# Performance work log

Measured on AMD Instinct MI355X. Metric: run time of the kernel, lower is better.

Reference implementation:

```python
import jax, jax.numpy as jnp
import numpy as np

D_IN, D, P, H, DH, DFF, L = 3072, 1024, 36, 8, 128, 2048, 6
SCALE = np.float32(1.0 / np.sqrt(DH))
# leave-one-out index matrix: row i lists all patch indices except i -> (36, 35)
LOO_IDX = jnp.asarray(np.array([[j for j in range(P) if j != i] for i in range(P)], dtype=np.int32))


def _ln(x, g, b, eps=1e-5):
    m = jnp.mean(x, axis=-1, keepdims=True)
    v = jnp.var(x, axis=-1, keepdims=True)
    return (x - m) / jnp.sqrt(v + eps) * g + b


def setup_inputs() -> dict:
    key = jax.random.key(0)
    ks = jax.random.split(key, 16)
    w = lambda k, shape: jax.random.normal(k, shape, jnp.float32) * 0.02
    return {
        "x": jax.random.normal(ks[0], (128, P, D_IN), jnp.float32),
        "ln0_g": jnp.ones((D_IN,), jnp.float32), "ln0_b": jnp.zeros((D_IN,), jnp.float32),
        "Wred": w(ks[1], (D, D_IN)), "bred": jnp.zeros((D,), jnp.float32),
        "h0_w1": w(ks[2], (64, D)), "h0_b1": jnp.zeros((64,), jnp.float32),
        "h0_w2": w(ks[3], (1, 64)), "h0_b2": jnp.zeros((1,), jnp.float32),
        "temperature": jnp.ones((1,), jnp.float32) * 0.07,
        "Wqkv": w(ks[4], (L, 3 * D, D)), "bqkv": jnp.zeros((L, 3 * D), jnp.float32),
        "Wo": w(ks[5], (L, D, D)), "bo": jnp.zeros((L, D), jnp.float32),
        "ln1_g": jnp.ones((L, D), jnp.float32), "ln1_b": jnp.zeros((L, D), jnp.float32),
        "W1": w(ks[6], (L, DFF, D)), "b1": jnp.zeros((L, DFF), jnp.float32),
        "W2": w(ks[7], (L, D, DFF)), "b2": jnp.zeros((L, D), jnp.float32),
        "ln2_g": jnp.ones((L, D), jnp.float32), "ln2_b": jnp.zeros((L, D), jnp.float32),
        "lnf_g": jnp.ones((D,), jnp.float32), "lnf_b": jnp.zeros((D,), jnp.float32),
    }


def reference(x, ln0_g, ln0_b, Wred, bred, h0_w1, h0_b1, h0_w2, h0_b2, temperature,
              Wqkv, bqkv, Wo, bo, ln1_g, ln1_b, W1, b1, W2, b2, ln2_g, ln2_b, lnf_g, lnf_b):
    B = x.shape[0]
    # dim_reduce (dropout is identity at inference)
    xr = jax.nn.gelu(_ln(x, ln0_g, ln0_b) @ Wred.T + bred, approximate=False)  # (B,P,D)

    # Leave-one-out attention maps. H0 is a pointwise (kernel_size=1) stack,
    # so each position's score is independent: compute once, then gather the
    h1 = jax.nn.gelu(jnp.einsum('bpc,oc->bpo', xr, h0_w1) + h0_b1, approximate=False)  # (B,P,64)
    full = jnp.einsum('bpo,uo->bpu', h1, h0_w2)[..., 0] + h0_b2[0]                      # (B,P)
    attention_maps = jax.nn.sigmoid(full[:, LOO_IDX] / temperature[0])                  # (B,P,P-1)

    # Pre-norm transformer encoder (PyTorch norm_first=True, relu FFN, no final encoder norm)
    y = xr
    for l in range(L):
        qkv = _ln(y, ln1_g[l], ln1_b[l]) @ Wqkv[l].T + bqkv[l]  # (B,P,3D)
        q, k, v = jnp.split(qkv, 3, axis=-1)
        q = q.reshape(B, P, H, DH).transpose(0, 2, 1, 3)
        k = k.reshape(B, P, H, DH).transpose(0, 2, 1, 3)
        v = v.reshape(B, P, H, DH).transpose(0, 2, 1, 3)
        attn = jax.nn.softmax(jnp.einsum('bhqd,bhkd->bhqk', q, k) * SCALE, axis=-1)
        o = jnp.einsum('bhqk,bhkd->bhqd', attn, v).transpose(0, 2, 1, 3).reshape(B, P, D)
        y = y + o @ Wo[l].T + bo[l]
        f = jax.nn.relu(_ln(y, ln2_g[l], ln2_b[l]) @ W1[l].T + b1[l])
        y = y + f @ W2[l].T + b2[l]

    return _ln(y, lnf_g, lnf_b), attention_maps
```

## Files before the change

kernel.cpp:

```cpp
#include <hip/hip_runtime.h>
#include <hip/hip_bf16.h>

typedef unsigned short u16;
typedef unsigned int u32;
typedef __bf16 bf16x8 __attribute__((ext_vector_type(8)));
typedef float f32x4 __attribute__((ext_vector_type(4)));

#define DEV static __device__ __forceinline__
#define GPTR(p) (const __attribute__((address_space(1))) u32*)(p)
#define LPTR(p) (__attribute__((address_space(3))) u32*)(p)

DEV float bf2f(u16 u) { return __uint_as_float((u32)u << 16); }
DEV u16 f2bf(float f) {
  u32 x = __float_as_uint(f);
  x += 0x7fffu + ((x >> 16) & 1u);
  return (u16)(x >> 16);
}
DEV float gelu_f(float x) { return 0.5f * x * (1.0f + erff(x * 0.70710678118654752440f)); }

__global__ void cvt_k(const float* __restrict__ in, u16* __restrict__ out, int n4) {
  int i = blockIdx.x * 256 + threadIdx.x;
  if (i < n4) {
    float4 v = ((const float4*)in)[i];
    ushort4 o;
    o.x = f2bf(v.x); o.y = f2bf(v.y); o.z = f2bf(v.z); o.w = f2bf(v.w);
    ((ushort4*)out)[i] = o;
  }
}

__global__ void w1t_k(const float* __restrict__ w1, float* __restrict__ w1t) {
  int i = blockIdx.x * 256 + threadIdx.x;
  if (i < 64 * 1024) {
    int o = i >> 10, c = i & 1023;
    w1t[c * 64 + o] = w1[i];
  }
}

template<int DIM, int OUTM>
__global__ __launch_bounds__(256) void ln_k(const float* __restrict__ in,
                                            const float* __restrict__ g,
                                            const float* __restrict__ b,
                                            void* __restrict__ outp) {
  constexpr int NV = DIM / 1024;
  const int row = blockIdx.x, tid = threadIdx.x;
  const float* x = in + (size_t)row * DIM;
  float4 v[NV];
  float s = 0.f, s2 = 0.f;
#pragma unroll
  for (int i = 0; i < NV; ++i) {
    v[i] = ((const float4*)x)[tid + i * 256];
    s += v[i].x + v[i].y + v[i].z + v[i].w;
    s2 += v[i].x * v[i].x + v[i].y * v[i].y + v[i].z * v[i].z + v[i].w * v[i].w;
  }
  __shared__ float red[8];
#pragma unroll
  for (int off = 32; off; off >>= 1) { s += __shfl_down(s, off); s2 += __shfl_down(s2, off); }
  if ((tid & 63) == 0) { red[(tid >> 6) * 2] = s; red[(tid >> 6) * 2 + 1] = s2; }
  __syncthreads();
  s = red[0] + red[2] + red[4] + red[6];
  s2 = red[1] + red[3] + red[5] + red[7];
  const float mean = s / DIM;
  const float rstd = rsqrtf(s2 / DIM - mean * mean + 1e-5f);
#pragma unroll
  for (int i = 0; i < NV; ++i) {
    const int c4 = tid + i * 256;
    float4 gv = ((const float4*)g)[c4];
    float4 bv = ((const float4*)b)[c4];
    float o0 = (v[i].x - mean) * rstd * gv.x + bv.x;
    float o1 = (v[i].y - mean) * rstd * gv.y + bv.y;
    float o2 = (v[i].z - mean) * rstd * gv.z + bv.z;
    float o3 = (v[i].w - mean) * rstd * gv.w + bv.w;
    if (OUTM == 0) {
      ushort4 u4;
      u4.x = f2bf(o0); u4.y = f2bf(o1); u4.z = f2bf(o2); u4.w = f2bf(o3);
      ((ushort4*)outp)[(size_t)row * (DIM / 4) + c4] = u4;
    } else {
      ((float4*)outp)[(size_t)row * (DIM / 4) + c4] = make_float4(o0, o1, o2, o3);
    }
  }
}

template<int EPI, int BN>
__global__ __launch_bounds__(512, 4) void gemm_bt(const u16* __restrict__ A,
                                                  const u16* __restrict__ B,
                                                  const float* __restrict__ bias,
                                                  float* __restrict__ Cf,
                                                  u16* __restrict__ Cb,
                                                  int N, int K, int nx) {
  constexpr int WC = BN / 32;
  constexpr int MR = (128 * WC / 8) / 16;
  __shared__ u16 As[2][128 * 64];
  __shared__ u16 Bs[2][BN * 64];
  const int tid = threadIdx.x;
  const int nwg = gridDim.x;
  const int bid = blockIdx.x;
  const int swz = (bid & 7) * (nwg >> 3) + (bid >> 3);
  const int by = swz / nx, bx = swz - by * nx;
  const int brow = by * 128, bcol = bx * BN;
  const int lane = tid & 63, w = tid >> 6;
  const int wr = (w / WC) * (MR * 16), wc = (w % WC) * 32;
  const int fr = lane & 15, fg = lane >> 4;
  const int swb = (fr & 7) << 4;
  const int ldr = lane >> 3;
  const int lc8 = lane & 7;
  const int cs8 = (lc8 ^ ldr) * 8;

  const u16* Ab = A + (size_t)(brow + ldr) * K + cs8;
  const u16* Bb = B + (size_t)(bcol + ldr) * K + cs8;

  f32x4 acc[MR][2];
  const f32x4 z = {0.f, 0.f, 0.f, 0.f};
#pragma unroll
  for (int m = 0; m < MR; ++m) { acc[m][0] = z; acc[m][1] = z; }

  auto stage = [&](int kt, int buf) {
    const int k0 = kt << 6;
#pragma unroll
    for (int i = 0; i < 2; ++i) {
      const int c = i * 8 + w;
      __builtin_amdgcn_global_load_lds(GPTR(Ab + (size_t)c * 8 * K + k0),
                                       LPTR(&As[buf][c * 512 + lane * 8]), 16, 0, 0);
    }
#pragma unroll
    for (int i = 0; i < BN / 64; ++i) {
      const int c = i * 8 + w;
      __builtin_amdgcn_global_load_lds(GPTR(Bb + (size_t)c * 8 * K + k0),
                                       LPTR(&Bs[buf][c * 512 + lane * 8]), 16, 0, 0);
    }
  };

  stage(0, 0);
  const int nkt = K >> 6;
  for (int kt = 0; kt < nkt; ++kt) {
    const int buf = kt & 1;
    asm volatile("s_waitcnt vmcnt(0)" ::: "memory");
    __builtin_amdgcn_s_barrier();
    __builtin_amdgcn_sched_barrier(0);
    if (kt + 1 < nkt) stage(kt + 1, buf ^ 1);
    const char* Asb = (const char*)&As[buf][0];
    const char* Bsb = (const char*)&Bs[buf][0];
    __builtin_amdgcn_s_setprio(1);
#pragma unroll
    for (int ks = 0; ks < 2; ++ks) {
      bf16x8 af[MR], bfr[2];
      const int cb = (ks * 64 + fg * 16) ^ swb;
#pragma unroll
      for (int m = 0; m < MR; ++m)
        af[m] = *(const bf16x8*)(Asb + (wr + m * 16 + fr) * 128 + cb);
#pragma unroll
      for (int n = 0; n < 2; ++n)
        bfr[n] = *(const bf16x8*)(Bsb + (wc + n * 16 + fr) * 128 + cb);
#pragma unroll
      for (int m = 0; m < MR; ++m)
#pragma unroll
        for (int n = 0; n < 2; ++n)
          acc[m][n] = __builtin_amdgcn_mfma_f32_16x16x32_bf16(af[m], bfr[n], acc[m][n], 0, 0, 0);
    }
    __builtin_amdgcn_s_setprio(0);
  }

#pragma unroll
  for (int n = 0; n < 2; ++n) {
    const int col = bcol + wc + n * 16 + fr;
    const float bv = bias[col];
#pragma unroll
    for (int m = 0; m < MR; ++m) {
      const int row0 = brow + wr + m * 16 + fg * 4;
#pragma unroll
      for (int j = 0; j < 4; ++j) {
        float v = acc[m][n][j] + bv;
        const size_t idx = (size_t)(row0 + j) * N + col;
        if (EPI == 0) Cf[idx] = gelu_f(v);
        else if (EPI == 1) Cb[idx] = f2bf(v);
        else if (EPI == 2) Cf[idx] = Cf[idx] + v;
        else Cb[idx] = f2bf(fmaxf(v, 0.f));
      }
    }
  }
}

__global__ __launch_bounds__(256) void attn_k(const u16* __restrict__ qkv, u16* __restrict__ o) {
  constexpr int LDQ = 136;
  __shared__ u16 Q[36 * LDQ], Kk[36 * LDQ], V[36 * LDQ];
  __shared__ float S[36][38];
  const int tid = threadIdx.x;
  const int b = blockIdx.x >> 3, h = blockIdx.x & 7;
  const size_t base = (size_t)b * 36 * 3072 + h * 128;
  for (int i = tid; i < 36 * 16; i += 256) {
    const int r = i >> 4, c = (i & 15) << 3;
    const size_t src = base + (size_t)r * 3072 + c;
    *(uint4*)&Q[r * LDQ + c] = *(const uint4*)&qkv[src];
    *(uint4*)&Kk[r * LDQ + c] = *(const uint4*)&qkv[src + 1024];
    *(uint4*)&V[r * LDQ + c] = *(const uint4*)&qkv[src + 2048];
  }
  __syncthreads();
  for (int i = tid; i < 36 * 36; i += 256) {
    const int r = i / 36, c = i - r * 36;
    float s = 0.f;
    for (int d = 0; d < 128; ++d) s += bf2f(Q[r * LDQ + d]) * bf2f(Kk[c * LDQ + d]);
    S[r][c] = s * 0.08838834764831845f;
  }
  __syncthreads();
  if (tid < 36) {
    float mx = -1e30f;
    for (int c = 0; c < 36; ++c) mx = fmaxf(mx, S[tid][c]);
    float sum = 0.f;
    for (int c = 0; c < 36; ++c) { float e = expf(S[tid][c] - mx); S[tid][c] = e; sum += e; }
    const float inv = 1.f / sum;
    for (int c = 0; c < 36; ++c) S[tid][c] *= inv;
  }
  __syncthreads();
  for (int i = tid; i < 36 * 16; i += 256) {
    const int r = i >> 4, d0 = (i & 15) << 3;
    float s[8] = {0.f, 0.f, 0.f, 0.f, 0.f, 0.f, 0.f, 0.f};
    for (int j = 0; j < 36; ++j) {
      const float p = S[r][j];
#pragma unroll
      for (int e = 0; e < 8; ++e) s[e] += p * bf2f(V[j * LDQ + d0 + e]);
    }
    uint4 pk;
    pk.x = (u32)f2bf(s[0]) | ((u32)f2bf(s[1]) << 16);
    pk.y = (u32)f2bf(s[2]) | ((u32)f2bf(s[3]) << 16);
    pk.z = (u32)f2bf(s[4]) | ((u32)f2bf(s[5]) << 16);
    pk.w = (u32)f2bf(s[6]) | ((u32)f2bf(s[7]) << 16);
    *(uint4*)&o[(size_t)(b * 36 + r) * 1024 + h * 128 + d0] = pk;
  }
}

__global__ __launch_bounds__(256) void h0_k(const float* __restrict__ xr,
                                            const float* __restrict__ w1t,
                                            const float* __restrict__ b1,
                                            const float* __restrict__ w2,
                                            const float* __restrict__ b2v,
                                            float* __restrict__ full) {
  __shared__ float xs[1024];
  __shared__ float hp[4][64];
  const int token = blockIdx.x, tid = threadIdx.x;
  ((float4*)xs)[tid] = ((const float4*)(xr + (size_t)token * 1024))[tid];
  __syncthreads();
  const int w = tid >> 6, lane = tid & 63;
  float s = 0.f;
  const int c0 = w * 256;
  for (int c = c0; c < c0 + 256; ++c) s += xs[c] * w1t[c * 64 + lane];
  hp[w][lane] = s;
  __syncthreads();
  if (tid < 64) {
    float h = hp[0][tid] + hp[1][tid] + hp[2][tid] + hp[3][tid] + b1[tid];
    h = gelu_f(h);
    float v = h * w2[tid];
#pragma unroll
    for (int off = 32; off; off >>= 1) v += __shfl_down(v, off);
    if (tid == 0) full[token] = v + b2v[0];
  }
}

__global__ void am2_k(const float* __restrict__ full, const float* __restrict__ temp,
                      float* __restrict__ out) {
  const int i = blockIdx.x * 256 + threadIdx.x;
  if (i < 128 * 36 * 35) {
    const int j = i % 35;
    const int t = i / 35;
    const int p = t % 36;
    const int b = t / 36;
    const int col = j + (j >= p ? 1 : 0);
    const float v = full[b * 36 + col] / temp[0];
    out[i] = 1.f / (1.f + expf(-v));
  }
}

extern "C" void kernel_launch(void* const* d_in, const int* in_sizes, int n_in,
                              void* d_out, int out_size, void* d_ws, size_t ws_size,
                              hipStream_t stream) {
  const float* x     = (const float*)d_in[0];
  const float* ln0_g = (const float*)d_in[1];
  const float* ln0_b = (const float*)d_in[2];
  const float* Wred  = (const float*)d_in[3];
  const float* bred  = (const float*)d_in[4];
  const float* h0_w1 = (const float*)d_in[5];
  const float* h0_b1 = (const float*)d_in[6];
  const float* h0_w2 = (const float*)d_in[7];
  const float* h0_b2 = (const float*)d_in[8];
  const float* temp  = (const float*)d_in[9];
  const float* Wqkv  = (const float*)d_in[10];
  const float* bqkv  = (const float*)d_in[11];
  const float* Wo    = (const float*)d_in[12];
  const float* bo    = (const float*)d_in[13];
  const float* ln1_g = (const float*)d_in[14];
  const float* ln1_b = (const float*)d_in[15];
  const float* W1    = (const float*)d_in[16];
  const float* b1    = (const float*)d_in[17];
  const float* W2    = (const float*)d_in[18];
  const float* b2    = (const float*)d_in[19];
  const float* ln2_g = (const float*)d_in[20];
  const float* ln2_b = (const float*)d_in[21];
  const float* lnf_g = (const float*)d_in[22];
  const float* lnf_b = (const float*)d_in[23];

  char* ws = (char*)d_ws;
  size_t off = 0;
  auto alloc = [&](size_t bytes) -> void* {
    void* p = ws + off;
    off += (bytes + 255) & ~(size_t)255;
    return p;
  };
  u16* WredB  = (u16*)alloc((size_t)1024 * 3072 * 2);
  u16* WqkvB  = (u16*)alloc((size_t)6 * 3072 * 1024 * 2);
  u16* WoB    = (u16*)alloc((size_t)6 * 1024 * 1024 * 2);
  u16* W1B    = (u16*)alloc((size_t)6 * 2048 * 1024 * 2);
  u16* W2B    = (u16*)alloc((size_t)6 * 1024 * 2048 * 2);
  float* w1t  = (float*)alloc((size_t)1024 * 64 * 4);
  float* yb   = (float*)alloc((size_t)4608 * 1024 * 4);
  u16* big    = (u16*)alloc((size_t)4608 * 3072 * 2);
  u16* nbuf   = (u16*)alloc((size_t)4608 * 1024 * 2);
  float* fullb = (float*)alloc((size_t)4608 * 4);

  auto cvt = [&](const float* src, u16* dst, size_t n) {
    int n4 = (int)(n / 4);
    cvt_k<<<(n4 + 255) / 256, 256, 0, stream>>>(src, dst, n4);
  };
  cvt(Wred, WredB, (size_t)1024 * 3072);
  cvt(Wqkv, WqkvB, (size_t)6 * 3072 * 1024);
  cvt(Wo,   WoB,   (size_t)6 * 1024 * 1024);
  cvt(W1,   W1B,   (size_t)6 * 2048 * 1024);
  cvt(W2,   W2B,   (size_t)6 * 1024 * 2048);
  w1t_k<<<64 * 1024 / 256, 256, 0, stream>>>(h0_w1, w1t);

  ln_k<3072, 0><<<4608, 256, 0, stream>>>(x, ln0_g, ln0_b, big);
  gemm_bt<0, 64><<<16 * 36, 512, 0, stream>>>(big, WredB, bred, yb, nullptr, 1024, 3072, 16);
  h0_k<<<4608, 256, 0, stream>>>(yb, w1t, h0_b1, h0_w2, h0_b2, fullb);
  am2_k<<<(128 * 36 * 35 + 255) / 256, 256, 0, stream>>>(fullb, temp,
                                                         (float*)d_out + 4608 * 1024);

  for (int l = 0; l < 6; ++l) {
    ln_k<1024, 0><<<4608, 256, 0, stream>>>(yb, ln1_g + l * 1024, ln1_b + l * 1024, nbuf);
    gemm_bt<1, 128><<<24 * 36, 512, 0, stream>>>(nbuf, WqkvB + (size_t)l * 3072 * 1024,
                                                 bqkv + l * 3072, nullptr, big, 3072, 1024, 24);
    attn_k<<<128 * 8, 256, 0, stream>>>(big, nbuf);
    gemm_bt<2, 64><<<16 * 36, 512, 0, stream>>>(nbuf, WoB + (size_t)l * 1024 * 1024,
                                                bo + l * 1024, yb, nullptr, 1024, 1024, 16);
    ln_k<1024, 0><<<4608, 256, 0, stream>>>(yb, ln2_g + l * 1024, ln2_b + l * 1024, nbuf);
    gemm_bt<3, 128><<<16 * 36, 512, 0, stream>>>(nbuf, W1B + (size_t)l * 2048 * 1024,
                                                 b1 + l * 2048, nullptr, big, 2048, 1024, 16);
    gemm_bt<2, 64><<<16 * 36, 512, 0, stream>>>(big, W2B + (size_t)l * 1024 * 2048,
                                                b2 + l * 1024, yb, nullptr, 1024, 2048, 16);
  }
  ln_k<1024, 1><<<4608, 256, 0, stream>>>(yb, lnf_g, lnf_b, d_out);
}
```

Before: 1.227 ms.

## Triple-buffer GEMM LDS staging with two-tile prefetch and partial vmcnt waits

Replaces the double-buffered K loop in the bf16 MFMA GEMM with a three-slot LDS ring that prefetches two K-tiles ahead. The loop waits with a partial vmcnt so only the oldest tile must have landed. Global-to-LDS loads for tile t+2 are issued after the fragment reads and before the MFMAs, fenced by sched_barriers, so memory latency overlaps compute. It uses more LDS per block, which may reduce occupancy, and depends on exact vmcnt counting being correct.

```diff
diff --git a/kernel.cpp b/kernel.cpp
--- a/kernel.cpp
+++ b/kernel.cpp
@@ -87,76 +87,109 @@
                                                   float* __restrict__ Cf,
                                                   u16* __restrict__ Cb,
                                                   int N, int K, int nx) {
-  constexpr int WC = BN / 32;
-  constexpr int MR = (128 * WC / 8) / 16;
-  __shared__ u16 As[2][128 * 64];
-  __shared__ u16 Bs[2][BN * 64];
+  constexpr int MR = (BN == 128) ? 4 : 2;
+  constexpr int ASLOT = 128 * 64;
+  constexpr int BSLOT = BN * 64;
+  __shared__ u16 As[3][ASLOT];
+  __shared__ u16 Bs[3][BSLOT];
   const int tid = threadIdx.x;
-  const int nwg = gridDim.x;
-  const int bid = blockIdx.x;
+  const int nwg = gridDim.x, bid = blockIdx.x;
   const int swz = (bid & 7) * (nwg >> 3) + (bid >> 3);
   const int by = swz / nx, bx = swz - by * nx;
   const int brow = by * 128, bcol = bx * BN;
   const int lane = tid & 63, w = tid >> 6;
-  const int wr = (w / WC) * (MR * 16), wc = (w % WC) * 32;
+  const int wr = (BN == 128) ? ((w >> 2) * 64) : ((w >> 1) * 32);
+  const int wc = (BN == 128) ? ((w & 3) * 32) : ((w & 1) * 32);
   const int fr = lane & 15, fg = lane >> 4;
   const int swb = (fr & 7) << 4;
-  const int ldr = lane >> 3;
-  const int lc8 = lane & 7;
-  const int cs8 = (lc8 ^ ldr) * 8;
-
-  const u16* Ab = A + (size_t)(brow + ldr) * K + cs8;
-  const u16* Bb = B + (size_t)(bcol + ldr) * K + cs8;
+  const int srow = tid >> 3;
+  const int scol = ((tid & 7) ^ (srow & 7)) * 8;
+
+  const u16* Ag = A + (size_t)(brow + srow) * K + scol;
+  const u16* Bg = B + (size_t)(bcol + srow) * K + scol;
 
   f32x4 acc[MR][2];
   const f32x4 z = {0.f, 0.f, 0.f, 0.f};
 #pragma unroll
   for (int m = 0; m < MR; ++m) { acc[m][0] = z; acc[m][1] = z; }
 
-  auto stage = [&](int kt, int buf) {
-    const int k0 = kt << 6;
-#pragma unroll
-    for (int i = 0; i < 2; ++i) {
-      const int c = i * 8 + w;
-      __builtin_amdgcn_global_load_lds(GPTR(Ab + (size_t)c * 8 * K + k0),
-                                       LPTR(&As[buf][c * 512 + lane * 8]), 16, 0, 0);
-    }
-#pragma unroll
-    for (int i = 0; i < BN / 64; ++i) {
-      const int c = i * 8 + w;
-      __builtin_amdgcn_global_load_lds(GPTR(Bb + (size_t)c * 8 * K + k0),
-                                       LPTR(&Bs[buf][c * 512 + lane * 8]), 16, 0, 0);
-    }
-  };
-
-  stage(0, 0);
+  auto stageA = [&](int kt, int s, int h) {
+    __builtin_amdgcn_global_load_lds(GPTR(Ag + (size_t)h * 64 * K + (kt << 6)),
+                                     LPTR(&As[s][h * 4096 + tid * 8]), 16, 0, 0);
+  };
+  auto stageB = [&](int kt, int s, int h) {
+    __builtin_amdgcn_global_load_lds(GPTR(Bg + (size_t)h * 64 * K + (kt << 6)),
+                                     LPTR(&Bs[s][h * 4096 + tid * 8]), 16, 0, 0);
+  };
+  auto rdA = [&](int s, int m, int ks) -> bf16x8 {
+    const int rr = wr + m * 16 + fr;
+    return *(const bf16x8*)((const char*)&As[s][0] + rr * 128 + ((ks * 64 + fg * 16) ^ swb));
+  };
+  auto rdB = [&](int s, int n, int ks) -> bf16x8 {
+    const int rb = wc + n * 16 + fr;
+    return *(const bf16x8*)((const char*)&Bs[s][0] + rb * 128 + ((ks * 64 + fg * 16) ^ swb));
+  };
+
   const int nkt = K >> 6;
-  for (int kt = 0; kt < nkt; ++kt) {
-    const int buf = kt & 1;
-    asm volatile("s_waitcnt vmcnt(0)" ::: "memory");
+#pragma unroll
+  for (int t = 0; t < 2; ++t) {
+    stageA(t, t, 0); stageA(t, t, 1);
+    stageB(t, t, 0);
+    if (BN == 128) stageB(t, t, 1);
+  }
+  int s0 = 0, s2 = 2;
+
+  for (int t = 0; t < nkt; ++t) {
+    const bool pre = (t + 2 < nkt);
+    if (t == nkt - 1) asm volatile("s_waitcnt vmcnt(0)" ::: "memory");
+    else if constexpr (BN == 128) asm volatile("s_waitcnt vmcnt(4)" ::: "memory");
+    else asm volatile("s_waitcnt vmcnt(3)" ::: "memory");
     __builtin_amdgcn_s_barrier();
     __builtin_amdgcn_sched_barrier(0);
-    if (kt + 1 < nkt) stage(kt + 1, buf ^ 1);
-    const char* Asb = (const char*)&As[buf][0];
-    const char* Bsb = (const char*)&Bs[buf][0];
-    __builtin_amdgcn_s_setprio(1);
-#pragma unroll
-    for (int ks = 0; ks < 2; ++ks) {
-      bf16x8 af[MR], bfr[2];
-      const int cb = (ks * 64 + fg * 16) ^ swb;
-#pragma unroll
-      for (int m = 0; m < MR; ++m)
-        af[m] = *(const bf16x8*)(Asb + (wr + m * 16 + fr) * 128 + cb);
-#pragma unroll
-      for (int n = 0; n < 2; ++n)
-        bfr[n] = *(const bf16x8*)(Bsb + (wc + n * 16 + fr) * 128 + cb);
-#pragma unroll
-      for (int m = 0; m < MR; ++m)
-#pragma unroll
-        for (int n = 0; n < 2; ++n)
-          acc[m][n] = __builtin_amdgcn_mfma_f32_16x16x32_bf16(af[m], bfr[n], acc[m][n], 0, 0, 0);
+
+    if constexpr (BN == 128) {
+#pragma unroll
+      for (int ks = 0; ks < 2; ++ks) {
+        bf16x8 af[4], bf2r[2];
+#pragma unroll
+        for (int m = 0; m < 4; ++m) af[m] = rdA(s0, m, ks);
+#pragma unroll
+        for (int n = 0; n < 2; ++n) bf2r[n] = rdB(s0, n, ks);
+        if (pre) { stageA(t + 2, s2, ks); stageB(t + 2, s2, ks); }
+        __builtin_amdgcn_sched_barrier(0);
+        __builtin_amdgcn_s_setprio(1);
+#pragma unroll
+        for (int m = 0; m < 4; ++m)
+#pragma unroll
+          for (int n = 0; n < 2; ++n)
+            acc[m][n] = __builtin_amdgcn_mfma_f32_16x16x32_bf16(af[m], bf2r[n], acc[m][n], 0, 0, 0);
+        __builtin_amdgcn_s_setprio(0);
+        __builtin_amdgcn_sched_barrier(0);
+      }
+    } else {
+      bf16x8 af[2][2], bf2r[2][2];
+#pragma unroll
+      for (int ks = 0; ks < 2; ++ks) {
+#pragma unroll
+        for (int m = 0; m < 2; ++m) af[m][ks] = rdA(s0, m, ks);
+#pragma unroll
+        for (int n = 0; n < 2; ++n) bf2r[n][ks] = rdB(s0, n, ks);
+      }
+      if (pre) { stageA(t + 2, s2, 0); stageA(t + 2, s2, 1); stageB(t + 2, s2, 0); }
+      __builtin_amdgcn_sched_barrier(0);
+      __builtin_amdgcn_s_setprio(1);
+#pragma unroll
+      for (int ks = 0; ks < 2; ++ks)
+#pragma unroll
+        for (int m = 0; m < 2; ++m)
+#pragma unroll
+          for (int n = 0; n < 2; ++n)
+            acc[m][n] = __builtin_amdgcn_mfma_f32_16x16x32_bf16(af[m][ks], bf2r[n][ks], acc[m][n], 0, 0, 0);
+      __builtin_amdgcn_s_setprio(0);
+      __builtin_amdgcn_sched_barrier(0);
     }
-    __builtin_amdgcn_s_setprio(0);
+    s0 = (s0 == 2) ? 0 : s0 + 1;
+    s2 = (s2 == 2) ? 0 : s2 + 1;
   }
 
 #pragma unroll
```

New measurement: 1.457 ms. 18.7% more time.
